# Kernel tuning notes

Hardware: AMD Instinct MI355X
Metric: run time of the kernel (lower is better)

The kernel has to match this reference:

```python
import jax, jax.numpy as jnp
from jax import lax
import numpy as np

B, EMB, HEADS, LAYERS = 32, 512, 8, 4
SEQ_JD, TOK = 200, 50

def _mask_lg(S):
    # Faithful vectorization of CoKEModel.mask_lg (True = masked)
    m = np.ones((B, HEADS, S, S), dtype=bool)
    rows = np.arange(S)[:, None]
    cols = np.clip(rows - 5 + np.arange(10)[None, :], 0, S - 1)  # window=10, offset -5..4
    for h in range(6):  # local_len = 6 local-window heads
        m[:, h, rows, cols] = False
    m[0, 6:] = False          # global heads unmasked only for batch 0 (faithful to source)
    m[:, :, 0, :] = False     # CLS row attends everywhere
    return m

def _ln_free(x):
    # CoKEModel.layer_norm: no affine, eps=1e-12, rsqrt form
    mu = jnp.mean(x, axis=-1, keepdims=True)
    sx = x - mu
    v = jnp.mean(sx * sx, axis=-1, keepdims=True)
    return sx * jnp.sqrt(1.0 / (v + 1e-12))

def _ln(x, g, b):
    mu = jnp.mean(x, axis=-1, keepdims=True)
    sx = x - mu
    v = jnp.mean(sx * sx, axis=-1, keepdims=True)
    return sx / jnp.sqrt(v + 1e-5) * g + b

def _textcnn(tokens, emb, cws, cbs, fw, fb):
    e = emb[tokens]                        # (N, 50, 1024)
    x = jnp.transpose(e, (0, 2, 1))        # (N, 1024, 50): embed dim as channels
    pooled = []
    for W, b in zip(cws, cbs):             # W: (100, k, 1024)
        rhs = jnp.transpose(W, (0, 2, 1))  # (100, 1024, k)
        y = lax.conv_general_dilated(x, rhs, (1,), 'VALID', dimension_numbers=('NCH', 'OIH', 'NCH'))
        y = jax.nn.relu(y + b[None, :, None])
        pooled.append(jnp.max(y, axis=2))  # global max-pool over time
    return jnp.concatenate(pooled, axis=1) @ fw.T + fb   # (N, 512)

def _encoder(x, mask, wq, bq, wk, bk, wv, bv, wo, bo, l1g, l1b, fw1, fb1, fw2, fb2, l2g, l2b):
    Bb, S, D = x.shape
    dh = D // HEADS
    scale = 1.0 / (dh ** 0.5)
    for l in range(LAYERS):
        q = (x @ wq[l].T + bq[l]).reshape(Bb, S, HEADS, dh)
        k = (x @ wk[l].T + bk[l]).reshape(Bb, S, HEADS, dh)
        v = (x @ wv[l].T + bv[l]).reshape(Bb, S, HEADS, dh)
        s = jnp.einsum('bshd,bthd->bhst', q, k) * scale
        s = jnp.where(mask, -1e9, s)
        a = jax.nn.softmax(s, axis=-1)
        c = jnp.einsum('bhst,bthd->bshd', a, v).reshape(Bb, S, D)
        x = _ln(x + c @ wo[l].T + bo[l], l1g[l], l1b[l])
        h = jax.nn.relu(x @ fw1[l].T + fb1[l])
        x = _ln(x + h @ fw2[l].T + fb2[l], l2g[l], l2b[l])
    return x

def _contrastive(im, s, margin=0.02):
    sc = im @ s.T
    d = jnp.diag(sc)
    cs = jnp.maximum(margin + sc - d[:, None], 0.0)
    ci = jnp.maximum(margin + sc - d[None, :], 0.0)
    eye = jnp.eye(sc.shape[0], dtype=bool)
    cs = jnp.where(eye, 0.0, cs)
    ci = jnp.where(eye, 0.0, ci)
    return jnp.sum(cs) + jnp.sum(ci)

def _forward(floats, src, mask101, mask200):
    (user_info, label_similarity, emb_tc, cw1, cb1, cw2, cb2, cw3, cb3, tfw, tfb,
     wq, bq, wk, bk, wv, bv, wo, bo, l1g, l1b, fw1, fb1, fw2, fb2, l2g, l2b,
     fc1w, fc1b, fc2w, fc2b, fc3w, fc3b, fc4w, fc4b, pscale, pbias) = floats
    cws, cbs = (cw1, cw2, cw3), (cb1, cb2, cb3)
    enc = (wq, bq, wk, bk, wv, bv, wo, bo, l1g, l1b, fw1, fb1, fw2, fb2, l2g, l2b)

    # ---- first pass: first 100 JDs + global CLS token ----
    s1 = _textcnn(src[:, :100].reshape(-1, TOK), emb_tc, cws, cbs, tfw, tfb).reshape(B, 100, EMB)
    s1 = _ln_free(s1)
    s1 = jnp.concatenate([jnp.zeros((B, 1, EMB), s1.dtype), s1], axis=1)  # (B, 101, EMB)
    p = _encoder(s1, mask101, *enc)
    p = jax.nn.gelu(p @ fc1w.T + fc1b, approximate=False)
    p = _ln_free(p)
    p = p * pscale[:, :p.shape[1]] + pbias[:, :p.shape[1]]
    p = p @ fc2w.T + fc2b                      # (B, 101, 204)
    cls_e, tok = p[:, :1], p[:, 1:]
    P = tok @ fc3w.T + fc3b                    # (B, 100, 204)
    clsIII = cls_e @ fc3w.T + fc3b             # (B, 1, 204)
    SLl = jnp.einsum('bsm,bsn->bmn', P, P)     # P^T @ P
    SL_hat = label_similarity[None] + 0.4 * SLl
    outIII = jnp.squeeze(clsIII @ SL_hat, axis=1)  # (B, 204)

    # ---- second pass: all 200 JDs ----
    s2 = _textcnn(src.reshape(-1, TOK), emb_tc, cws, cbs, tfw, tfb).reshape(B, SEQ_JD, EMB)
    s2 = _ln_free(s2)
    ap = _encoder(s2, mask200, *enc)
    ap = jax.nn.gelu(ap @ fc1w.T + fc1b, approximate=False)
    ap = _ln_free(ap)
    ap = ap * pscale[:, :SEQ_JD] + pbias[:, :SEQ_JD]
    p1 = ap @ fc2w.T + fc2b                    # (B, 200, 204)

    nn_ = SEQ_JD // 100  # = 2 neighbors
    eps = 1e-6
    skl_rows, seuc_rows = [], []
    for i in range(nn_):
        # NOTE: faithful to source slicing bug: [i : (i+1)*100]
        c1 = jax.nn.softmax(jnp.mean(p1[:, i:(i + 1) * 100], axis=1), axis=-1)
        a1 = jax.nn.softmax(jnp.mean(ap[:, i:(i + 1) * 100], axis=1), axis=-1)
        rk, re = [], []
        for j in range(nn_):
            c2 = jax.nn.softmax(jnp.mean(p1[:, j:(j + 1) * 100], axis=1), axis=-1)
            a2 = jax.nn.softmax(jnp.mean(ap[:, j:(j + 1) * 100], axis=1), axis=-1)
            rk.append(jnp.sum((c1 + eps) * jnp.log((c1 + eps) / (c2 + eps)), axis=-1))
            re.append(jnp.sqrt(jnp.sum((a1 - a2) ** 2, axis=-1) + 1e-12))
        skl_rows.append(jnp.stack(rk, axis=-1))
        seuc_rows.append(jnp.stack(re, axis=-1))
    skl = jnp.stack(skl_rows, axis=1).reshape(B, -1) * 10.0
    seuc = jnp.stack(seuc_rows, axis=1).reshape(B, -1)
    skl = jax.nn.softmax(skl, axis=-1)
    seuc = jax.nn.softmax(seuc, axis=-1)
    loss_sims = jnp.mean(jnp.sum((skl + eps) * jnp.log((skl + eps) / (seuc + eps)), axis=-1))

    cls4m = jnp.squeeze(cls_e, axis=1)
    user4m = user_info @ fc4w.T + fc4b
    nrm = lambda x: x / jnp.maximum(jnp.linalg.norm(x, axis=1, keepdims=True), 1e-12)
    match = _contrastive(nrm(cls4m), nrm(user4m))

    return (jax.nn.softmax(outIII, axis=-1),
            jax.nn.softmax(cls_e, axis=-1),
            loss_sims * 100000.0,
            match * 0.01)

def setup_inputs():
    key = jax.random.key(0)
    kit = iter(jax.random.split(key, 48))
    def nrm(shape, s=0.02):
        return jax.random.normal(next(kit), shape, jnp.float32) * s
    d = {}
    d['src'] = jax.random.randint(next(kit), (B, SEQ_JD, TOK), 0, 20000)
    d['user_info'] = nrm((B, 142), 1.0)
    d['label_similarity'] = nrm((204, 204))
    d['emb_tc'] = nrm((20000, 1024)).at[0].set(0.0)  # padding_idx=0 row zeroed
    d['cw1'], d['cb1'] = nrm((100, 1, 1024)), jnp.zeros((100,), jnp.float32)
    d['cw2'], d['cb2'] = nrm((100, 2, 1024)), jnp.zeros((100,), jnp.float32)
    d['cw3'], d['cb3'] = nrm((100, 3, 1024)), jnp.zeros((100,), jnp.float32)
    d['tfw'], d['tfb'] = nrm((512, 300)), jnp.zeros((512,), jnp.float32)
    d['wq'], d['bq'] = nrm((LAYERS, EMB, EMB)), jnp.zeros((LAYERS, EMB), jnp.float32)
    d['wk'], d['bk'] = nrm((LAYERS, EMB, EMB)), jnp.zeros((LAYERS, EMB), jnp.float32)
    d['wv'], d['bv'] = nrm((LAYERS, EMB, EMB)), jnp.zeros((LAYERS, EMB), jnp.float32)
    d['wo'], d['bo'] = nrm((LAYERS, EMB, EMB)), jnp.zeros((LAYERS, EMB), jnp.float32)
    d['l1g'], d['l1b'] = jnp.ones((LAYERS, EMB), jnp.float32), jnp.zeros((LAYERS, EMB), jnp.float32)
    d['fw1'], d['fb1'] = nrm((LAYERS, 2048, EMB)), jnp.zeros((LAYERS, 2048), jnp.float32)
    d['fw2'], d['fb2'] = nrm((LAYERS, EMB, 2048)), jnp.zeros((LAYERS, EMB), jnp.float32)
    d['l2g'], d['l2b'] = jnp.ones((LAYERS, EMB), jnp.float32), jnp.zeros((LAYERS, EMB), jnp.float32)
    d['fc1w'], d['fc1b'] = nrm((EMB, EMB)), jnp.zeros((EMB,), jnp.float32)
    d['fc2w'], d['fc2b'] = nrm((204, EMB)), jnp.zeros((204,), jnp.float32)
    d['fc3w'], d['fc3b'] = nrm((204, 204)), jnp.zeros((204,), jnp.float32)
    d['fc4w'], d['fc4b'] = nrm((204, 142)), jnp.zeros((204,), jnp.float32)
    d['pscale'] = jnp.ones((B, 300, EMB), jnp.float32)
    d['pbias'] = jnp.zeros((B, 300, EMB), jnp.float32)
    d['mask101'] = jnp.asarray(_mask_lg(101))
    d['mask200'] = jnp.asarray(_mask_lg(SEQ_JD))
    return d

def reference(src, user_info, label_similarity, emb_tc, cw1, cb1, cw2, cb2, cw3, cb3, tfw, tfb, wq, bq, wk, bk, wv, bv, wo, bo, l1g, l1b, fw1, fb1, fw2, fb2, l2g, l2b, fc1w, fc1b, fc2w, fc2b, fc3w, fc3b, fc4w, fc4b, pscale, pbias, mask101, mask200):
    floats = (user_info, label_similarity, emb_tc, cw1, cb1, cw2, cb2, cw3, cb3, tfw, tfb,
              wq, bq, wk, bk, wv, bv, wo, bo, l1g, l1b, fw1, fb1, fw2, fb2, l2g, l2b,
              fc1w, fc1b, fc2w, fc2b, fc3w, fc3b, fc4w, fc4b, pscale, pbias)
    return _forward(floats, src, mask101, mask200)
```

## Files before the change

### kernel.cpp

```cpp
#include <hip/hip_runtime.h>
#include <math.h>

#define EMB 512
#define HEADS 8
#define NLAYERS 4
#define NB 32
#define SEQ 200
#define TOKN 50
#define DH 64
#define FFND 2048
#define NCLS 204
#define VC 640
#define KD 1024
#define CCH 8
#define CROWS (6400/CCH)
#define CM (CROWS*TOKN)
#define MSEG 16
#define CMT ((CM + 127) / 128)
#define CNT (VC / 128)
#define CT  (CMT * CNT)

typedef __attribute__((ext_vector_type(8))) short v8s;
typedef __attribute__((ext_vector_type(4))) float v4f;
typedef unsigned short ushort_t;

__device__ __forceinline__ ushort_t f2bu(float f){
  unsigned u = __float_as_uint(f);
  return (ushort_t)((u + 0x7FFFu + ((u >> 16) & 1u)) >> 16);
}
__device__ __forceinline__ float bu2f(ushort_t u){
  return __uint_as_float(((unsigned)u) << 16);
}

__device__ __forceinline__ int xcd_swz(int lin, int nwg){
  int xcd = lin & 7, idx = lin >> 3;
  int q = nwg >> 3, r = nwg & 7;
  return ((xcd < r) ? xcd * (q + 1) : r * (q + 1) + (xcd - r) * q) + idx;
}

__device__ __forceinline__ float block_reduce(float v, float* red, int nwaves, bool domax){
  int tid = threadIdx.x;
  #pragma unroll
  for (int o = 32; o > 0; o >>= 1){
    float t = __shfl_down(v, o, 64);
    v = domax ? fmaxf(v, t) : (v + t);
  }
  __syncthreads();
  if ((tid & 63) == 0) red[tid >> 6] = v;
  __syncthreads();
  float r = red[0];
  for (int i = 1; i < nwaves; i++) r = domax ? fmaxf(r, red[i]) : (r + red[i]);
  return r;
}

__global__ void prep_w_kernel(const float* __restrict__ cw1, const float* __restrict__ cw2,
                              const float* __restrict__ cw3, ushort_t* __restrict__ Wb){
  int idx4 = blockIdx.x * 256 + threadIdx.x;
  if (idx4 >= VC * KD / 4) return;
  int row = idx4 >> 8;
  int k = (idx4 & 255) * 4;
  float4 v = make_float4(0.f, 0.f, 0.f, 0.f);
  const float* s = nullptr;
  if (row < 100)      s = cw1 + (size_t)row * KD;
  else if (row < 200) s = cw2 + (size_t)((row - 100) * 2 + 0) * KD;
  else if (row < 300) s = cw2 + (size_t)((row - 200) * 2 + 1) * KD;
  else if (row < 400) s = cw3 + (size_t)((row - 300) * 3 + 0) * KD;
  else if (row < 500) s = cw3 + (size_t)((row - 400) * 3 + 1) * KD;
  else if (row < 600) s = cw3 + (size_t)((row - 500) * 3 + 2) * KD;
  if (s) v = *(const float4*)(s + k);
  ushort4 o;
  o.x = f2bu(v.x); o.y = f2bu(v.y); o.z = f2bu(v.z); o.w = f2bu(v.w);
  *(ushort4*)(Wb + (size_t)row * KD + k) = o;
}

__global__ void prep_embbf_kernel(const float* __restrict__ emb, ushort_t* __restrict__ embb){
  size_t i4 = ((size_t)blockIdx.x * 256 + threadIdx.x) * 4;
  if (i4 >= 20000ULL * KD) return;
  float4 f = *(const float4*)(emb + i4);
  ushort4 o;
  o.x = f2bu(f.x); o.y = f2bu(f.y); o.z = f2bu(f.z); o.w = f2bu(f.w);
  *(ushort4*)(embb + i4) = o;
}

__global__ void prep_tfwT_kernel(const float* __restrict__ tfw, float* __restrict__ tfwT){
  int idx = blockIdx.x * 256 + threadIdx.x;
  if (idx >= 300 * EMB) return;
  int j = idx >> 9, o = idx & 511;
  tfwT[(size_t)j * EMB + o] = tfw[(size_t)o * 300 + j];
}

__global__ void split_kernel(const float* __restrict__ src, ushort_t* __restrict__ hi,
                             ushort_t* __restrict__ lo, int n){
  int i4 = (blockIdx.x * 256 + threadIdx.x) * 4;
  if (i4 >= n) return;
  float4 f = *(const float4*)(src + i4);
  float x[4] = {f.x, f.y, f.z, f.w};
  ushort4 h, l;
  ushort_t hh[4], ll[4];
  #pragma unroll
  for (int e = 0; e < 4; e++){
    unsigned u = __float_as_uint(x[e]);
    float hf = __uint_as_float(u & 0xFFFF0000u);
    hh[e] = (ushort_t)(u >> 16);
    ll[e] = f2bu(x[e] - hf);
  }
  h.x=hh[0]; h.y=hh[1]; h.z=hh[2]; h.w=hh[3];
  l.x=ll[0]; l.y=ll[1]; l.z=ll[2]; l.w=ll[3];
  *(ushort4*)(hi + i4) = h;
  *(ushort4*)(lo + i4) = l;
}

__global__ void qkvbias_kernel(const float* __restrict__ bq, const float* __restrict__ bk,
                               const float* __restrict__ bv, float* __restrict__ bqkv){
  int l = blockIdx.x;
  for (int j = threadIdx.x; j < 1536; j += 256){
    float v;
    if (j < 512) v = bq[l * 512 + j];
    else if (j < 1024) v = bk[l * 512 + j - 512];
    else v = bv[l * 512 + j - 1024];
    bqkv[l * 1536 + j] = v;
  }
}

__global__ __launch_bounds__(256, 4) void conv_gemm_kernel(
    const int* __restrict__ tok, const ushort_t* __restrict__ embb,
    const ushort_t* __restrict__ Wb, ushort_t* __restrict__ Cout, int Mc)
{
  __shared__ ushort_t Al[128][40];
  __shared__ ushort_t Bl[128][40];
  const int tid = threadIdx.x;
  const int t = xcd_swz(blockIdx.x, CT);
  const int n0 = (t % CNT) * 128;
  const int m0 = (t / CNT) * 128;
  const int wave = tid >> 6, lane = tid & 63;
  const int wm = (wave >> 1) * 64, wn = (wave & 1) * 64;
  const int lcol = lane & 15, lq = lane >> 4;

  v4f acc[4][4];
  #pragma unroll
  for (int i = 0; i < 4; i++)
    #pragma unroll
    for (int j = 0; j < 4; j++) acc[i][j] = (v4f){0.f, 0.f, 0.f, 0.f};

  const int srow = tid >> 1, skh = (tid & 1) * 16;
  const int am = m0 + srow;
  const ushort_t* aep = (am < Mc) ? (embb + (size_t)tok[am] * KD + skh) : nullptr;
  const ushort_t* bep = Wb + (size_t)(n0 + srow) * KD + skh;

  for (int k0 = 0; k0 < KD; k0 += 32){
    uint4 a0 = make_uint4(0,0,0,0), a1 = make_uint4(0,0,0,0);
    if (aep){
      a0 = *(const uint4*)(aep + k0);
      a1 = *(const uint4*)(aep + k0 + 8);
    }
    *(uint4*)&Al[srow][skh]     = a0;
    *(uint4*)&Al[srow][skh + 8] = a1;
    uint4 b0 = *(const uint4*)(bep + k0);
    uint4 b1 = *(const uint4*)(bep + k0 + 8);
    *(uint4*)&Bl[srow][skh]     = b0;
    *(uint4*)&Bl[srow][skh + 8] = b1;
    __syncthreads();

    v8s af[4];
    #pragma unroll
    for (int mi = 0; mi < 4; mi++)
      af[mi] = *(const v8s*)&Al[wm + mi*16 + lcol][lq*8];
    #pragma unroll
    for (int ni = 0; ni < 4; ni++){
      v8s bf = *(const v8s*)&Bl[wn + ni*16 + lcol][lq*8];
      #pragma unroll
      for (int mi = 0; mi < 4; mi++)
        acc[mi][ni] = __builtin_amdgcn_mfma_f32_16x16x32_bf16(af[mi], bf, acc[mi][ni], 0, 0, 0);
    }
    __syncthreads();
  }

  #pragma unroll
  for (int ni = 0; ni < 4; ni++){
    int n = n0 + wn + ni*16 + lcol;
    #pragma unroll
    for (int mi = 0; mi < 4; mi++){
      int mbase = m0 + wm + mi*16 + lq*4;
      #pragma unroll
      for (int rg = 0; rg < 4; rg++){
        int m = mbase + rg;
        if (m < Mc) Cout[(size_t)m * VC + n] = f2bu(acc[mi][ni][rg]);
      }
    }
  }
}

__global__ __launch_bounds__(256, 2) void pool_fc_kernel(
    const ushort_t* __restrict__ Cc, const float* __restrict__ tfwT,
    const float* __restrict__ cb1, const float* __restrict__ cb2,
    const float* __restrict__ cb3, const float* __restrict__ tfb,
    float* __restrict__ basep)
{
  __shared__ ushort_t Sg[VC][54];
  __shared__ float pooled[304];
  __shared__ float red[8];
  const int tid = threadIdx.x;
  const int r = blockIdx.x;

  const unsigned* cr = (const unsigned*)(Cc + (size_t)r * TOKN * VC);
  for (int p = 0; p < TOKN; p++){
    for (int t = tid; t < VC/2; t += 256){
      unsigned u = cr[p * (VC/2) + t];
      Sg[2*t][p]   = (ushort_t)(u & 0xFFFFu);
      Sg[2*t+1][p] = (ushort_t)(u >> 16);
    }
  }
  __syncthreads();

  for (int c = tid; c < 300; c += 256){
    float mv = -1e30f;
    if (c < 100){
      float bb = cb1[c];
      for (int p = 0; p < 50; p++) mv = fmaxf(mv, bu2f(Sg[c][p]) + bb);
    } else if (c < 200){
      int o = c - 100; float bb = cb2[o];
      for (int p = 0; p < 49; p++)
        mv = fmaxf(mv, bu2f(Sg[100 + o][p]) + bu2f(Sg[200 + o][p + 1]) + bb);
    } else {
      int o = c - 200; float bb = cb3[o];
      for (int p = 0; p < 48; p++)
        mv = fmaxf(mv, bu2f(Sg[300 + o][p]) + bu2f(Sg[400 + o][p + 1]) + bu2f(Sg[500 + o][p + 2]) + bb);
    }
    pooled[c] = fmaxf(mv, 0.f);
  }
  __syncthreads();

  float v0 = tfb[tid], v1 = tfb[tid + 256];
  for (int j = 0; j < 300; j++){
    float pj = pooled[j];
    v0 = fmaf(pj, tfwT[(size_t)j * EMB + tid], v0);
    v1 = fmaf(pj, tfwT[(size_t)j * EMB + tid + 256], v1);
  }
  float tot = block_reduce(v0 + v1, red, 4, false);
  float mu = tot * (1.f / 512.f);
  float s0 = v0 - mu, s1 = v1 - mu;
  float var = block_reduce(s0 * s0 + s1 * s1, red, 4, false) * (1.f / 512.f);
  float sc = sqrtf(1.f / (var + 1e-12f));
  basep[(size_t)r * EMB + tid] = s0 * sc;
  basep[(size_t)r * EMB + tid + 256] = s1 * sc;
}

__global__ __launch_bounds__(256, 3) void gemm_mfma_pre_kernel(
    const float* __restrict__ A, const ushort_t* __restrict__ Whi,
    const ushort_t* __restrict__ Wlo, const float* __restrict__ bias,
    float* __restrict__ C, int M, int N, int K, int ldc, int act, int mt, int nt)
{
  __shared__ ushort_t Ahi[128][40];
  __shared__ ushort_t Alo[128][40];
  __shared__ ushort_t Bhi[128][40];
  __shared__ ushort_t Blo[128][40];

  const int tid = threadIdx.x;
  const int t = xcd_swz(blockIdx.x, mt * nt);
  const int n0 = (t % nt) * 128, m0 = (t / nt) * 128;
  const int wave = tid >> 6, lane = tid & 63;
  const int wm = (wave >> 1) * 64, wn = (wave & 1) * 64;
  const int lcol = lane & 15, lq = lane >> 4;

  v4f acc[4][4];
  #pragma unroll
  for (int i = 0; i < 4; i++)
    #pragma unroll
    for (int j = 0; j < 4; j++) acc[i][j] = (v4f){0.f, 0.f, 0.f, 0.f};

  const int srow = tid >> 1;
  const int skh  = (tid & 1) * 16;
  const int am = m0 + srow, bn = n0 + srow;
  const bool mok = (am < M), nok = (bn < N);
  const float* ap = A + (size_t)am * K + skh;
  const ushort_t* bph = Whi + (size_t)bn * K + skh;
  const ushort_t* bpl = Wlo + (size_t)bn * K + skh;

  for (int k0 = 0; k0 < K; k0 += 32){
    bool kfull = (k0 + 32 <= K);
    {
      float av[16];
      if (mok && kfull){
        #pragma unroll
        for (int q = 0; q < 4; q++){
          float4 f = *(const float4*)(ap + k0 + q*4);
          av[q*4+0]=f.x; av[q*4+1]=f.y; av[q*4+2]=f.z; av[q*4+3]=f.w;
        }
      } else {
        #pragma unroll
        for (int e = 0; e < 16; e++){
          int k = k0 + skh + e;
          av[e] = (mok && k < K) ? ap[k0 + e] : 0.f;
        }
      }
      uint4 uh[2], ul[2];
      #pragma unroll
      for (int h = 0; h < 2; h++){
        unsigned hw[8], lw[8];
        #pragma unroll
        for (int e = 0; e < 8; e++){
          float x = av[h*8+e];
          unsigned u = __float_as_uint(x);
          float hf = __uint_as_float(u & 0xFFFF0000u);
          hw[e] = u >> 16;
          lw[e] = f2bu(x - hf);
        }
        uh[h] = make_uint4(hw[0]|(hw[1]<<16), hw[2]|(hw[3]<<16), hw[4]|(hw[5]<<16), hw[6]|(hw[7]<<16));
        ul[h] = make_uint4(lw[0]|(lw[1]<<16), lw[2]|(lw[3]<<16), lw[4]|(lw[5]<<16), lw[6]|(lw[7]<<16));
      }
      *(uint4*)&Ahi[srow][skh]     = uh[0];
      *(uint4*)&Ahi[srow][skh + 8] = uh[1];
      *(uint4*)&Alo[srow][skh]     = ul[0];
      *(uint4*)&Alo[srow][skh + 8] = ul[1];
    }
    {
      uint4 h0 = make_uint4(0,0,0,0), h1 = h0, l0 = h0, l1 = h0;
      if (nok && kfull){
        h0 = *(const uint4*)(bph + k0);
        h1 = *(const uint4*)(bph + k0 + 8);
        l0 = *(const uint4*)(bpl + k0);
        l1 = *(const uint4*)(bpl + k0 + 8);
      } else if (nok){
        ushort_t he[16], le[16];
        #pragma unroll
        for (int e = 0; e < 16; e++){
          int k = k0 + skh + e;
          he[e] = (k < K) ? bph[k0 + e] : (ushort_t)0;
          le[e] = (k < K) ? bpl[k0 + e] : (ushort_t)0;
        }
        h0 = *(uint4*)&he[0]; h1 = *(uint4*)&he[8];
        l0 = *(uint4*)&le[0]; l1 = *(uint4*)&le[8];
      }
      *(uint4*)&Bhi[srow][skh]     = h0;
      *(uint4*)&Bhi[srow][skh + 8] = h1;
      *(uint4*)&Blo[srow][skh]     = l0;
      *(uint4*)&Blo[srow][skh + 8] = l1;
    }
    __syncthreads();

    v8s ah[4], al[4];
    #pragma unroll
    for (int mi = 0; mi < 4; mi++){
      ah[mi] = *(const v8s*)&Ahi[wm + mi*16 + lcol][lq*8];
      al[mi] = *(const v8s*)&Alo[wm + mi*16 + lcol][lq*8];
    }
    #pragma unroll
    for (int ni = 0; ni < 4; ni++){
      v8s bh = *(const v8s*)&Bhi[wn + ni*16 + lcol][lq*8];
      v8s bl = *(const v8s*)&Blo[wn + ni*16 + lcol][lq*8];
      #pragma unroll
      for (int mi = 0; mi < 4; mi++){
        acc[mi][ni] = __builtin_amdgcn_mfma_f32_16x16x32_bf16(ah[mi], bh, acc[mi][ni], 0, 0, 0);
        acc[mi][ni] = __builtin_amdgcn_mfma_f32_16x16x32_bf16(al[mi], bh, acc[mi][ni], 0, 0, 0);
        acc[mi][ni] = __builtin_amdgcn_mfma_f32_16x16x32_bf16(ah[mi], bl, acc[mi][ni], 0, 0, 0);
      }
    }
    __syncthreads();
  }

  #pragma unroll
  for (int ni = 0; ni < 4; ni++){
    int n = n0 + wn + ni*16 + lcol;
    if (n >= N) continue;
    float bv = bias[n];
    #pragma unroll
    for (int mi = 0; mi < 4; mi++){
      int mbase = m0 + wm + mi*16 + lq*4;
      #pragma unroll
      for (int rg = 0; rg < 4; rg++){
        int m = mbase + rg;
        if (m >= M) continue;
        float v = acc[mi][ni][rg] + bv;
        if (act == 1) v = fmaxf(v, 0.f);
        else if (act == 2) v = 0.5f * v * (1.f + erff(v * 0.70710678118654752f));
        C[(size_t)m * ldc + n] = v;
      }
    }
  }
}

__global__ __launch_bounds__(256, 4) void gemm_mfma_pre64_kernel(
    const float* __restrict__ A, const ushort_t* __restrict__ Whi,
    const ushort_t* __restrict__ Wlo, const float* __restrict__ bias,
    float* __restrict__ C, int M, int N, int K, int ldc, int act, int mt, int nt)
{
  __shared__ ushort_t Ahi[128][40];
  __shared__ ushort_t Alo[128][40];
  __shared__ ushort_t Bhi[64][40];
  __shared__ ushort_t Blo[64][40];

  const int tid = threadIdx.x;
  const int t = xcd_swz(blockIdx.x, mt * nt);
  const int n0 = (t % nt) * 64, m0 = (t / nt) * 128;
  const int wave = tid >> 6, lane = tid & 63;
  const int wm = (wave >> 1) * 64, wn = (wave & 1) * 32;
  const int lcol = lane & 15, lq = lane >> 4;

  v4f acc[4][2];
  #pragma unroll
  for (int i = 0; i < 4; i++)
    #pragma unroll
    for (int j = 0; j < 2; j++) acc[i][j] = (v4f){0.f, 0.f, 0.f, 0.f};

  const int srow = tid >> 1;
  const int skh  = (tid & 1) * 16;
  const int am = m0 + srow;
  const bool mok = (am < M);
  const float* ap = A + (size_t)am * K + skh;
  const int brow = tid >> 2;
  const int bkq  = (tid & 3) * 8;
  const int bn = n0 + brow;
  const bool nok = (bn < N);
  const ushort_t* bph = Whi + (size_t)bn * K + bkq;
  const ushort_t* bpl = Wlo + (size_t)bn * K + bkq;

  for (int k0 = 0; k0 < K; k0 += 32){
    bool kfull = (k0 + 32 <= K);
    {
      float av[16];
      if (mok && kfull){
        #pragma unroll
        for (int q = 0; q < 4; q++){
          float4 f = *(const float4*)(ap + k0 + q*4);
          av[q*4+0]=f.x; av[q*4+1]=f.y; av[q*4+2]=f.z; av[q*4+3]=f.w;
        }
      } else {
        #pragma unroll
        for (int e = 0; e < 16; e++){
          int k = k0 + skh + e;
          av[e] = (mok && k < K) ? ap[k0 + e] : 0.f;
        }
      }
      uint4 uh[2], ul[2];
      #pragma unroll
      for (int h = 0; h < 2; h++){
        unsigned hw[8], lw[8];
        #pragma unroll
        for (int e = 0; e < 8; e++){
          float x = av[h*8+e];
          unsigned u = __float_as_uint(x);
          float hf = __uint_as_float(u & 0xFFFF0000u);
          hw[e] = u >> 16;
          lw[e] = f2bu(x - hf);
        }
        uh[h] = make_uint4(hw[0]|(hw[1]<<16), hw[2]|(hw[3]<<16), hw[4]|(hw[5]<<16), hw[6]|(hw[7]<<16));
        ul[h] = make_uint4(lw[0]|(lw[1]<<16), lw[2]|(lw[3]<<16), lw[4]|(lw[5]<<16), lw[6]|(lw[7]<<16));
      }
      *(uint4*)&Ahi[srow][skh]     = uh[0];
      *(uint4*)&Ahi[srow][skh + 8] = uh[1];
      *(uint4*)&Alo[srow][skh]     = ul[0];
      *(uint4*)&Alo[srow][skh + 8] = ul[1];
    }
    {
      uint4 h0 = make_uint4(0,0,0,0), l0 = h0;
      if (nok && kfull){
        h0 = *(const uint4*)(bph + k0);
        l0 = *(const uint4*)(bpl + k0);
      } else if (nok){
        ushort_t he[8], le[8];
        #pragma unroll
        for (int e = 0; e < 8; e++){
          int k = k0 + bkq + e;
          he[e] = (k < K) ? bph[k0 + e] : (ushort_t)0;
          le[e] = (k < K) ? bpl[k0 + e] : (ushort_t)0;
        }
        h0 = *(uint4*)&he[0];
        l0 = *(uint4*)&le[0];
      }
      *(uint4*)&Bhi[brow][bkq] = h0;
      *(uint4*)&Blo[brow][bkq] = l0;
    }
    __syncthreads();

    v8s ah[4], al[4];
    #pragma unroll
    for (int mi = 0; mi < 4; mi++){
      ah[mi] = *(const v8s*)&Ahi[wm + mi*16 + lcol][lq*8];
      al[mi] = *(const v8s*)&Alo[wm + mi*16 + lcol][lq*8];
    }
    #pragma unroll
    for (int ni = 0; ni < 2; ni++){
      v8s bh = *(const v8s*)&Bhi[wn + ni*16 + lcol][lq*8];
      v8s bl = *(const v8s*)&Blo[wn + ni*16 + lcol][lq*8];
      #pragma unroll
      for (int mi = 0; mi < 4; mi++){
        acc[mi][ni] = __builtin_amdgcn_mfma_f32_16x16x32_bf16(ah[mi], bh, acc[mi][ni], 0, 0, 0);
        acc[mi][ni] = __builtin_amdgcn_mfma_f32_16x16x32_bf16(al[mi], bh, acc[mi][ni], 0, 0, 0);
        acc[mi][ni] = __builtin_amdgcn_mfma_f32_16x16x32_bf16(ah[mi], bl, acc[mi][ni], 0, 0, 0);
      }
    }
    __syncthreads();
  }

  #pragma unroll
  for (int ni = 0; ni < 2; ni++){
    int n = n0 + wn + ni*16 + lcol;
    if (n >= N) continue;
    float bv = bias[n];
    #pragma unroll
    for (int mi = 0; mi < 4; mi++){
      int mbase = m0 + wm + mi*16 + lq*4;
      #pragma unroll
      for (int rg = 0; rg < 4; rg++){
        int m = mbase + rg;
        if (m >= M) continue;
        float v = acc[mi][ni][rg] + bv;
        if (act == 1) v = fmaxf(v, 0.f);
        else if (act == 2) v = 0.5f * v * (1.f + erff(v * 0.70710678118654752f));
        C[(size_t)m * ldc + n] = v;
      }
    }
  }
}

__global__ __launch_bounds__(256, 2) void gemm_mfma_kernel(
    const float* __restrict__ A, const float* __restrict__ W,
    const float* __restrict__ bias, float* __restrict__ C,
    int M, int N, int K, int ldc, int act)
{
  __shared__ ushort_t Ahi[128][40];
  __shared__ ushort_t Alo[128][40];
  __shared__ ushort_t Bhi[128][40];
  __shared__ ushort_t Blo[128][40];

  const int tid = threadIdx.x;
  const int m0 = blockIdx.y * 128, n0 = blockIdx.x * 128;
  const int wave = tid >> 6, lane = tid & 63;
  const int wm = (wave >> 1) * 64, wn = (wave & 1) * 64;
  const int lcol = lane & 15, lq = lane >> 4;

  v4f acc[4][4];
  #pragma unroll
  for (int i = 0; i < 4; i++)
    #pragma unroll
    for (int j = 0; j < 4; j++) acc[i][j] = (v4f){0.f, 0.f, 0.f, 0.f};

  const int srow = tid >> 1;
  const int skh  = (tid & 1) * 16;

  for (int k0 = 0; k0 < K; k0 += 32){
    {
      float av[16];
      int m = m0 + srow;
      const float* ap = A + (size_t)m * K + k0 + skh;
      bool mok = (m < M);
      if (mok && (k0 + 32 <= K)){
        #pragma unroll
        for (int q = 0; q < 4; q++){
          float4 f = ((const float4*)ap)[q];
          av[q*4+0]=f.x; av[q*4+1]=f.y; av[q*4+2]=f.z; av[q*4+3]=f.w;
        }
      } else {
        #pragma unroll
        for (int e = 0; e < 16; e++){
          int k = k0 + skh + e;
          av[e] = (mok && k < K) ? ap[e] : 0.f;
        }
      }
      uint4 uh[2], ul[2];
      #pragma unroll
      for (int h = 0; h < 2; h++){
        unsigned hw[8], lw[8];
        #pragma unroll
        for (int e = 0; e < 8; e++){
          float x = av[h*8+e];
          unsigned u = __float_as_uint(x);
          float hf = __uint_as_float(u & 0xFFFF0000u);
          hw[e] = u >> 16;
          lw[e] = f2bu(x - hf);
        }
        uh[h] = make_uint4(hw[0]|(hw[1]<<16), hw[2]|(hw[3]<<16), hw[4]|(hw[5]<<16), hw[6]|(hw[7]<<16));
        ul[h] = make_uint4(lw[0]|(lw[1]<<16), lw[2]|(lw[3]<<16), lw[4]|(lw[5]<<16), lw[6]|(lw[7]<<16));
      }
      *(uint4*)&Ahi[srow][skh]     = uh[0];
      *(uint4*)&Ahi[srow][skh + 8] = uh[1];
      *(uint4*)&Alo[srow][skh]     = ul[0];
      *(uint4*)&Alo[srow][skh + 8] = ul[1];
    }
    {
      float bv[16];
      int n = n0 + srow;
      const float* bp = W + (size_t)n * K + k0 + skh;
      bool nok = (n < N);
      if (nok && (k0 + 32 <= K)){
        #pragma unroll
        for (int q = 0; q < 4; q++){
          float4 f = ((const float4*)bp)[q];
          bv[q*4+0]=f.x; bv[q*4+1]=f.y; bv[q*4+2]=f.z; bv[q*4+3]=f.w;
        }
      } else {
        #pragma unroll
        for (int e = 0; e < 16; e++){
          int k = k0 + skh + e;
          bv[e] = (nok && k < K) ? bp[e] : 0.f;
        }
      }
      uint4 uh[2], ul[2];
      #pragma unroll
      for (int h = 0; h < 2; h++){
        unsigned hw[8], lw[8];
        #pragma unroll
        for (int e = 0; e < 8; e++){
          float x = bv[h*8+e];
          unsigned u = __float_as_uint(x);
          float hf = __uint_as_float(u & 0xFFFF0000u);
          hw[e] = u >> 16;
          lw[e] = f2bu(x - hf);
        }
        uh[h] = make_uint4(hw[0]|(hw[1]<<16), hw[2]|(hw[3]<<16), hw[4]|(hw[5]<<16), hw[6]|(hw[7]<<16));
        ul[h] = make_uint4(lw[0]|(lw[1]<<16), lw[2]|(lw[3]<<16), lw[4]|(lw[5]<<16), lw[6]|(lw[7]<<16));
      }
      *(uint4*)&Bhi[srow][skh]     = uh[0];
      *(uint4*)&Bhi[srow][skh + 8] = uh[1];
      *(uint4*)&Blo[srow][skh]     = ul[0];
      *(uint4*)&Blo[srow][skh + 8] = ul[1];
    }
    __syncthreads();

    v8s ah[4], al[4];
    #pragma unroll
    for (int mi = 0; mi < 4; mi++){
      ah[mi] = *(const v8s*)&Ahi[wm + mi*16 + lcol][lq*8];
      al[mi] = *(const v8s*)&Alo[wm + mi*16 + lcol][lq*8];
    }
    #pragma unroll
    for (int ni = 0; ni < 4; ni++){
      v8s bh = *(const v8s*)&Bhi[wn + ni*16 + lcol][lq*8];
      v8s bl = *(const v8s*)&Blo[wn + ni*16 + lcol][lq*8];
      #pragma unroll
      for (int mi = 0; mi < 4; mi++){
        acc[mi][ni] = __builtin_amdgcn_mfma_f32_16x16x32_bf16(ah[mi], bh, acc[mi][ni], 0, 0, 0);
        acc[mi][ni] = __builtin_amdgcn_mfma_f32_16x16x32_bf16(al[mi], bh, acc[mi][ni], 0, 0, 0);
        acc[mi][ni] = __builtin_amdgcn_mfma_f32_16x16x32_bf16(ah[mi], bl, acc[mi][ni], 0, 0, 0);
      }
    }
    __syncthreads();
  }

  #pragma unroll
  for (int ni = 0; ni < 4; ni++){
    int n = n0 + wn + ni*16 + lcol;
    if (n >= N) continue;
    float bv = bias[n];
    #pragma unroll
    for (int mi = 0; mi < 4; mi++){
      int mbase = m0 + wm + mi*16 + lq*4;
      #pragma unroll
      for (int rg = 0; rg < 4; rg++){
        int m = mbase + rg;
        if (m >= M) continue;
        float v = acc[mi][ni][rg] + bv;
        if (act == 1) v = fmaxf(v, 0.f);
        else if (act == 2) v = 0.5f * v * (1.f + erff(v * 0.70710678118654752f));
        C[(size_t)m * ldc + n] = v;
      }
    }
  }
}

__global__ __launch_bounds__(256) void gemm_kernel(
    const float* __restrict__ A, const float* __restrict__ W,
    const float* __restrict__ bias, float* __restrict__ C,
// ... 303 lines not shown
    }
    dst[c] = s;
  }
}

__global__ __launch_bounds__(256) void means_final_kernel(
    const float* __restrict__ part, float* __restrict__ mp, float* __restrict__ ma)
{
  const int bi = blockIdx.x;
  const int i = bi & 1;
  const float icnt = (i == 0) ? (1.f / 100.f) : (1.f / 199.f);
  for (int c = threadIdx.x; c < NCLS + EMB; c += 256){
    float s = 0.f;
    #pragma unroll
    for (int g = 0; g < MSEG; g++)
      s += part[((size_t)(bi * MSEG + g)) * 720 + c];
    if (c < NCLS) mp[(size_t)bi * NCLS + c] = s * icnt;
    else          ma[(size_t)bi * EMB + (c - NCLS)] = s * icnt;
  }
}

__global__ __launch_bounds__(64) void klfinal_kernel(
    const float* __restrict__ cbuf, const float* __restrict__ abuf, float* __restrict__ acc)
{
  const int b = blockIdx.x, lane = threadIdx.x;
  float rk[4], re[4];
  #pragma unroll
  for (int pr = 0; pr < 4; pr++){
    int i = pr >> 1, j = pr & 1;
    const float* c1 = cbuf + ((size_t)(b * 2 + i)) * NCLS;
    const float* c2 = cbuf + ((size_t)(b * 2 + j)) * NCLS;
    float s = 0.f;
    for (int n = lane; n < NCLS; n += 64){
      float x = c1[n] + 1e-6f, y = c2[n] + 1e-6f;
      s += x * logf(x / y);
    }
    #pragma unroll
    for (int o = 32; o > 0; o >>= 1) s += __shfl_down(s, o, 64);
    rk[pr] = __shfl(s, 0, 64);
    const float* a1 = abuf + ((size_t)(b * 2 + i)) * EMB;
    const float* a2 = abuf + ((size_t)(b * 2 + j)) * EMB;
    float s2 = 0.f;
    for (int n = lane; n < EMB; n += 64){
      float dd = a1[n] - a2[n];
      s2 += dd * dd;
    }
    #pragma unroll
    for (int o = 32; o > 0; o >>= 1) s2 += __shfl_down(s2, o, 64);
    re[pr] = sqrtf(__shfl(s2, 0, 64) + 1e-12f);
  }
  if (lane == 0){
    float sk[4], se[4];
    float mk = -INFINITY, me = -INFINITY;
    for (int p = 0; p < 4; p++){
      sk[p] = rk[p] * 10.f;
      mk = fmaxf(mk, sk[p]);
      se[p] = re[p];
      me = fmaxf(me, se[p]);
    }
    float ssk = 0.f, sse = 0.f;
    for (int p = 0; p < 4; p++){ sk[p] = expf(sk[p] - mk); ssk += sk[p]; se[p] = expf(se[p] - me); sse += se[p]; }
    float loss = 0.f;
    for (int p = 0; p < 4; p++){
      float x = sk[p] / ssk + 1e-6f, y = se[p] / sse + 1e-6f;
      loss += x * logf(x / y);
    }
    atomicAdd(acc, loss);
  }
}

__global__ void finalize_kernel(const float* __restrict__ acc, float* __restrict__ out){
  if (threadIdx.x == 0) out[13056] = acc[0] * (100000.f / 32.f);
}

extern "C" void kernel_launch(void* const* d_in, const int* in_sizes, int n_in,
                              void* d_out, int out_size, void* d_ws, size_t ws_size,
                              hipStream_t stream)
{
  (void)in_sizes; (void)n_in; (void)out_size;
  const int*   src  = (const int*)  d_in[0];
  const float* user_info = (const float*)d_in[1];
  const float* ls   = (const float*)d_in[2];
  const float* emb  = (const float*)d_in[3];
  const float* cw1  = (const float*)d_in[4];  const float* cb1 = (const float*)d_in[5];
  const float* cw2  = (const float*)d_in[6];  const float* cb2 = (const float*)d_in[7];
  const float* cw3  = (const float*)d_in[8];  const float* cb3 = (const float*)d_in[9];
  const float* tfw  = (const float*)d_in[10]; const float* tfb = (const float*)d_in[11];
  const float* wq   = (const float*)d_in[12]; const float* bq  = (const float*)d_in[13];
  const float* wk   = (const float*)d_in[14]; const float* bk  = (const float*)d_in[15];
  const float* wv   = (const float*)d_in[16]; const float* bv  = (const float*)d_in[17];
  const float* wo   = (const float*)d_in[18]; const float* bo  = (const float*)d_in[19];
  const float* l1g  = (const float*)d_in[20]; const float* l1b = (const float*)d_in[21];
  const float* fw1  = (const float*)d_in[22]; const float* fb1 = (const float*)d_in[23];
  const float* fw2  = (const float*)d_in[24]; const float* fb2 = (const float*)d_in[25];
  const float* l2g  = (const float*)d_in[26]; const float* l2b = (const float*)d_in[27];
  const float* fc1w = (const float*)d_in[28]; const float* fc1b= (const float*)d_in[29];
  const float* fc2w = (const float*)d_in[30]; const float* fc2b= (const float*)d_in[31];
  const float* fc3w = (const float*)d_in[32]; const float* fc3b= (const float*)d_in[33];
  const float* fc4w = (const float*)d_in[34]; const float* fc4b= (const float*)d_in[35];
  const float* pscale = (const float*)d_in[36];
  const float* pbias  = (const float*)d_in[37];
  float* out = (float*)d_out;
  float* ws = (float*)d_ws;

  size_t off = 0;
  auto alloc = [&](size_t n){ float* p = ws + off; off += ((n + 3) & ~(size_t)3); return p; };
  float* base = alloc(6400ULL * EMB);
  float* x1   = alloc((size_t)NB * 101 * EMB);
  float* qkv  = alloc(6400ULL * 1536);
  float* ctx  = alloc(6400ULL * EMB);
  float* proj = alloc(6400ULL * EMB);
  float* hb   = alloc(6400ULL * FFND);
  float* p2   = alloc(6400ULL * NCLS);
  float* clsE = alloc((size_t)NB * NCLS);
  float* tok  = alloc(3200ULL * NCLS);
  float* Pb   = alloc(3200ULL * NCLS);
  float* cls3 = alloc((size_t)NB * NCLS);
  float* SLh  = alloc((size_t)NB * NCLS * NCLS);
  float* o3   = alloc((size_t)NB * NCLS);
  float* u4   = alloc((size_t)NB * NCLS);
  float* imn  = alloc((size_t)NB * NCLS);
  float* sn   = alloc((size_t)NB * NCLS);
  float* mp   = alloc(64ULL * NCLS);
  float* ma   = alloc(64ULL * EMB);
  float* cbf  = alloc(64ULL * NCLS);
  float* abf  = alloc(64ULL * EMB);
  float* lacc = alloc(4);
  float* vmb  = alloc((size_t)NB * HEADS * DH);
  ushort_t* Wb = (ushort_t*)alloc((size_t)VC * KD / 2);
  float* tfwT = alloc(300ULL * EMB);
  float* bqkv = alloc(4ULL * 1536);
  ushort_t* embb = (ushort_t*)qkv;
  const size_t OQKV = 0, OWO = 3145728, OF1 = 4194304, OF2 = 8388608;
  const size_t OC1 = 12582912, OC2 = 12845056, OC3 = 12949504, WTOT = 12991120;
  ushort_t* WhiA = (ushort_t*)alloc((WTOT + 1) / 2);
  ushort_t* WloA = (ushort_t*)alloc((WTOT + 1) / 2);
  const bool presplit = (off * sizeof(float) <= ws_size);

  auto gemm_f32 = [&](const float* A, const float* W, const float* bi, float* C,
                      int M, int N, int K, int act){
    dim3 g((N + 63) / 64, (M + 63) / 64);
    gemm_kernel<<<g, 256, 0, stream>>>(A, W, bi, C, M, N, K, act);
  };
  auto gemm_fly = [&](const float* A, const float* W, const float* bi, float* C,
                      int M, int N, int K, int ldc, int act){
    dim3 g((N + 127) / 128, (M + 127) / 128);
    gemm_mfma_kernel<<<g, 256, 0, stream>>>(A, W, bi, C, M, N, K, ldc, act);
  };
  auto gemm_pre = [&](const float* A, size_t woff, const float* bi, float* C,
                      int M, int N, int K, int ldc, int act){
    int mt = (M + 127) / 128;
    if (N <= 512){
      int nt = (N + 63) / 64;
      gemm_mfma_pre64_kernel<<<mt * nt, 256, 0, stream>>>(
          A, WhiA + woff, WloA + woff, bi, C, M, N, K, ldc, act, mt, nt);
    } else {
      int nt = (N + 127) / 128;
      gemm_mfma_pre_kernel<<<mt * nt, 256, 0, stream>>>(
          A, WhiA + woff, WloA + woff, bi, C, M, N, K, ldc, act, mt, nt);
    }
  };
  auto split = [&](const float* srcw, size_t woff, int n){
    split_kernel<<<(n / 4 + 255) / 256, 256, 0, stream>>>(srcw, WhiA + woff, WloA + woff, n);
  };

  prep_w_kernel<<<(VC * KD / 4 + 255) / 256, 256, 0, stream>>>(cw1, cw2, cw3, Wb);
  prep_embbf_kernel<<<(int)((20000ULL * KD / 4 + 255) / 256), 256, 0, stream>>>(emb, embb);
  prep_tfwT_kernel<<<(300 * EMB + 255) / 256, 256, 0, stream>>>(tfw, tfwT);
  if (presplit){
    for (int l = 0; l < NLAYERS; l++){
      split(wq + (size_t)l * 262144, OQKV + (size_t)l * 786432,          262144);
      split(wk + (size_t)l * 262144, OQKV + (size_t)l * 786432 + 262144, 262144);
      split(wv + (size_t)l * 262144, OQKV + (size_t)l * 786432 + 524288, 262144);
      split(wo + (size_t)l * 262144, OWO + (size_t)l * 262144, 262144);
      split(fw1 + (size_t)l * 1048576, OF1 + (size_t)l * 1048576, 1048576);
      split(fw2 + (size_t)l * 1048576, OF2 + (size_t)l * 1048576, 1048576);
    }
    split(fc1w, OC1, 262144);
    split(fc2w, OC2, NCLS * EMB);
    split(fc3w, OC3, NCLS * NCLS);
    qkvbias_kernel<<<4, 256, 0, stream>>>(bq, bk, bv, bqkv);
  }

  for (int c = 0; c < CCH; c++){
    conv_gemm_kernel<<<CT, 256, 0, stream>>>(
        src + (size_t)c * CM, embb, Wb, (ushort_t*)hb, CM);
    pool_fc_kernel<<<CROWS, 256, 0, stream>>>(
        (ushort_t*)hb, tfwT, cb1, cb2, cb3, tfb, base + (size_t)c * CROWS * EMB);
  }
  buildx1_kernel<<<(NB * 101 * EMB + 255) / 256, 256, 0, stream>>>(base, x1);

  auto encoder = [&](float* x, int S){
    int M = NB * S;
    for (int l = 0; l < NLAYERS; l++){
      if (presplit){
        gemm_pre(x, OQKV + (size_t)l * 786432, bqkv + l * 1536, qkv, M, 1536, EMB, 1536, 0);
      } else {
        gemm_fly(x, wq + (size_t)l * EMB * EMB, bq + l * EMB, qkv,        M, EMB, EMB, 1536, 0);
        gemm_fly(x, wk + (size_t)l * EMB * EMB, bk + l * EMB, qkv + 512,  M, EMB, EMB, 1536, 0);
        gemm_fly(x, wv + (size_t)l * EMB * EMB, bv + l * EMB, qkv + 1024, M, EMB, EMB, 1536, 0);
      }
      vmean_kernel<<<NB * HEADS, 64, 0, stream>>>(qkv, vmb, S);
      attn_kernel<<<NB * HEADS * S, 64, 0, stream>>>(qkv, vmb, ctx, S);
      if (presplit) gemm_pre(ctx, OWO + (size_t)l * 262144, bo + l * EMB, proj, M, EMB, EMB, EMB, 0);
      else gemm_fly(ctx, wo + (size_t)l * EMB * EMB, bo + l * EMB, proj, M, EMB, EMB, EMB, 0);
      ln_kernel<<<M, 256, 0, stream>>>(proj, x, l1g + l * EMB, l1b + l * EMB, nullptr, nullptr, x, S, 1e-5f);
      if (presplit) gemm_pre(x, OF1 + (size_t)l * 1048576, fb1 + l * FFND, hb, M, FFND, EMB, FFND, 1);
      else gemm_fly(x, fw1 + (size_t)l * FFND * EMB, fb1 + l * FFND, hb, M, FFND, EMB, FFND, 1);
      if (presplit) gemm_pre(hb, OF2 + (size_t)l * 1048576, fb2 + l * EMB, proj, M, EMB, FFND, EMB, 0);
      else gemm_fly(hb, fw2 + (size_t)l * EMB * FFND, fb2 + l * EMB, proj, M, EMB, FFND, EMB, 0);
      ln_kernel<<<M, 256, 0, stream>>>(proj, x, l2g + l * EMB, l2b + l * EMB, nullptr, nullptr, x, S, 1e-5f);
    }
    if (presplit) gemm_pre(x, OC1, fc1b, ctx, M, EMB, EMB, EMB, 2);
    else gemm_fly(x, fc1w, fc1b, ctx, M, EMB, EMB, EMB, 2);
    ln_kernel<<<M, 256, 0, stream>>>(ctx, nullptr, nullptr, nullptr, pscale, pbias, ctx, S, 1e-12f);
    if (presplit) gemm_pre(ctx, OC2, fc2b, p2, M, NCLS, EMB, NCLS, 0);
    else gemm_fly(ctx, fc2w, fc2b, p2, M, NCLS, EMB, NCLS, 0);
  };

  encoder(x1, 101);
  extract_kernel<<<(NB * 101 * NCLS + 255) / 256, 256, 0, stream>>>(p2, clsE, tok);
  if (presplit) gemm_pre(tok, OC3, fc3b, Pb, 3200, NCLS, NCLS, NCLS, 0);
  else gemm_fly(tok, fc3w, fc3b, Pb, 3200, NCLS, NCLS, NCLS, 0);
  gemm_f32(clsE, fc3w, fc3b, cls3, NB, NCLS, NCLS, 0);
  slhat_kernel<<<NB * NCLS, 256, 0, stream>>>(Pb, ls, SLh);
  outIII_kernel<<<NB, 256, 0, stream>>>(cls3, SLh, o3);
  softmax_out_kernel<<<NB, 256, 0, stream>>>(o3, out, NCLS);
  softmax_out_kernel<<<NB, 256, 0, stream>>>(clsE, out + NB * NCLS, NCLS);
  gemm_f32(user_info, fc4w, fc4b, u4, NB, NCLS, 142, 0);
  normalize_kernel<<<64, 256, 0, stream>>>(clsE, u4, imn, sn);
  contrastive_kernel<<<1, 1024, 0, stream>>>(imn, sn, out);

  encoder(base, SEQ);
  zero_kernel<<<1, 64, 0, stream>>>(lacc);
  means_part_kernel<<<64 * MSEG, 256, 0, stream>>>(p2, ctx, hb);
  means_final_kernel<<<64, 256, 0, stream>>>(hb, mp, ma);
  softmax_out_kernel<<<64, 256, 0, stream>>>(mp, cbf, NCLS);
  softmax_out_kernel<<<64, 256, 0, stream>>>(ma, abf, EMB);
  klfinal_kernel<<<NB, 64, 0, stream>>>(cbf, abf, lacc);
  finalize_kernel<<<1, 64, 0, stream>>>(lacc, out);
}
```

Baseline: 5.287 ms.

## Add split-K with atomic accumulation to narrow-N presplit GEMM

For GEMMs with N≤512 and no activation, the K dimension is split into up to 8 slices, each handled by its own block. Partial results are combined into the output with fp32 atomicAdd, after a new kernel zeroes the output; only slice 0 adds the bias. The goal is more blocks and better CU occupancy for GEMMs whose tile count is small relative to the GPU, such as the output projection and the FFN down-projection. The cost is an extra zeroing pass, atomic write traffic, and non-deterministic summation order. The zeroing also assumes the output is contiguous with ldc equal to N.

```diff
diff --git a/kernel.cpp b/kernel.cpp
--- a/kernel.cpp
+++ b/kernel.cpp
@@ -122,6 +122,13 @@
   }
 }
 
+__global__ __launch_bounds__(256) void zerobuf_kernel(float* __restrict__ p, size_t n4){
+  size_t i = (size_t)blockIdx.x * 256 + threadIdx.x;
+  size_t stride = (size_t)gridDim.x * 256;
+  for (; i < n4; i += stride)
+    ((float4*)p)[i] = make_float4(0.f, 0.f, 0.f, 0.f);
+}
+
 __global__ __launch_bounds__(256, 4) void conv_gemm_kernel(
     const int* __restrict__ tok, const ushort_t* __restrict__ embb,
     const ushort_t* __restrict__ Wb, ushort_t* __restrict__ Cout, int Mc)
@@ -382,7 +389,7 @@
 __global__ __launch_bounds__(256, 4) void gemm_mfma_pre64_kernel(
     const float* __restrict__ A, const ushort_t* __restrict__ Whi,
     const ushort_t* __restrict__ Wlo, const float* __restrict__ bias,
-    float* __restrict__ C, int M, int N, int K, int ldc, int act, int mt, int nt)
+    float* __restrict__ C, int M, int N, int K, int ldc, int act, int mt, int nt, int ks)
 {
   __shared__ ushort_t Ahi[128][40];
   __shared__ ushort_t Alo[128][40];
@@ -390,8 +397,15 @@
   __shared__ ushort_t Blo[64][40];
 
   const int tid = threadIdx.x;
-  const int t = xcd_swz(blockIdx.x, mt * nt);
+  const int tiles = mt * nt;
+  const int t_ = xcd_swz(blockIdx.x, tiles * ks);
+  const int slice = t_ / tiles;
+  const int t = t_ % tiles;
   const int n0 = (t % nt) * 64, m0 = (t / nt) * 128;
+  const int kstep = ((K + 31) / 32 + ks - 1) / ks;
+  const int kb = slice * kstep * 32;
+  const int ke = min(K, kb + kstep * 32);
+  if (kb >= ke) return;
   const int wave = tid >> 6, lane = tid & 63;
   const int wm = (wave >> 1) * 64, wn = (wave & 1) * 32;
   const int lcol = lane & 15, lq = lane >> 4;
@@ -414,7 +428,7 @@
   const ushort_t* bph = Whi + (size_t)bn * K + bkq;
   const ushort_t* bpl = Wlo + (size_t)bn * K + bkq;
 
-  for (int k0 = 0; k0 < K; k0 += 32){
+  for (int k0 = kb; k0 < ke; k0 += 32){
     bool kfull = (k0 + 32 <= K);
     {
       float av[16];
@@ -496,7 +510,7 @@
   for (int ni = 0; ni < 2; ni++){
     int n = n0 + wn + ni*16 + lcol;
     if (n >= N) continue;
-    float bv = bias[n];
+    float bv = (ks == 1 || slice == 0) ? bias[n] : 0.f;
     #pragma unroll
     for (int mi = 0; mi < 4; mi++){
       int mbase = m0 + wm + mi*16 + lq*4;
@@ -505,9 +519,13 @@
         int m = mbase + rg;
         if (m >= M) continue;
         float v = acc[mi][ni][rg] + bv;
-        if (act == 1) v = fmaxf(v, 0.f);
-        else if (act == 2) v = 0.5f * v * (1.f + erff(v * 0.70710678118654752f));
-        C[(size_t)m * ldc + n] = v;
+        if (ks == 1){
+          if (act == 1) v = fmaxf(v, 0.f);
+          else if (act == 2) v = 0.5f * v * (1.f + erff(v * 0.70710678118654752f));
+          C[(size_t)m * ldc + n] = v;
+        } else {
+          atomicAdd(&C[(size_t)m * ldc + n], v);
+        }
       }
     }
   }
@@ -1117,8 +1135,18 @@
     int mt = (M + 127) / 128;
     if (N <= 512){
       int nt = (N + 63) / 64;
-      gemm_mfma_pre64_kernel<<<mt * nt, 256, 0, stream>>>(
-          A, WhiA + woff, WloA + woff, bi, C, M, N, K, ldc, act, mt, nt);
+      int tiles = mt * nt;
+      int ks = 1;
+      if (act == 0){
+        while (ks < 8 && tiles * ks * 2 <= 2048 && K / (ks * 2) >= 128) ks *= 2;
+      }
+      if (ks > 1){
+        size_t n4 = ((size_t)M * N) / 4;
+        int zg = (int)min((n4 + 255) / 256, (size_t)2048);
+        zerobuf_kernel<<<zg, 256, 0, stream>>>(C, n4);
+      }
+      gemm_mfma_pre64_kernel<<<tiles * ks, 256, 0, stream>>>(
+          A, WhiA + woff, WloA + woff, bi, C, M, N, K, ldc, act, mt, nt, ks);
     } else {
       int nt = (N + 127) / 128;
       gemm_mfma_pre_kernel<<<mt * nt, 256, 0, stream>>>(
```

Measured after the change: 5.308 ms. No clear change (+0.4%).
